# Kernel tuning notes

Measured on AMD Instinct MI355X. Metric: run time of the kernel, lower is better.

The kernel has to match this reference:

```python
import jax, jax.numpy as jnp
import numpy as np

B, S, D_IN, D_OUT = 2, 512, 512, 512
EPS = 1e-5  # torch F.layer_norm default


def _layer_norm_last(x):
    # torch F.layer_norm over last dim, no affine, biased variance
    mu = jnp.mean(x, axis=-1, keepdims=True)
    var = jnp.mean(jnp.square(x - mu), axis=-1, keepdims=True)
    return (x - mu) * jax.lax.rsqrt(var + EPS)


def setup_inputs() -> dict:
    key = jax.random.key(0)
    k_x, k_in, k_out, k_b = jax.random.split(key, 4)
    # torch Linear weights: shape (out_features, in_features), kaiming-uniform-ish scale
    lim = 1.0 / np.sqrt(D_IN)
    x = jax.random.normal(k_x, (B, S, D_IN), dtype=jnp.float32)
    W_in = jax.random.uniform(k_in, (D_IN, D_IN), minval=-lim, maxval=lim, dtype=jnp.float32)
    W_out = jax.random.uniform(k_out, (D_OUT, D_IN), minval=-lim, maxval=lim, dtype=jnp.float32)
    W_b = jax.random.uniform(k_b, (D_OUT, D_IN), minval=-lim, maxval=lim, dtype=jnp.float32)
    return {"x": x, "W_in": W_in, "W_out": W_out, "W_b": W_b}


def reference(x, W_in, W_out, W_b):
    # w1: [B,S,D_in], w2: [B,S,D_out]  (torch Linear: x @ W.T)
    w1 = jnp.einsum('bsd,ed->bse', x, W_in)
    w2 = jnp.einsum('bsd,ed->bse', x, W_out)
    # per-token rank-1 meta weight: [B,S,D_out,D_in]
    w = jnp.einsum('bsi,bsj->bsij', w2, w1)
    w = _layer_norm_last(w)  # normalize each row over in_features
    b = _layer_norm_last(jnp.einsum('bsd,ed->bse', x, W_b))  # [B,S,D_out]
    # batched mat-vec: [B,S,D_out]
    y = jnp.einsum('bsij,bsj->bsi', w, x) + b
    return y
```

## Files before the change

### kernel.cpp

```cpp
#include <hip/hip_runtime.h>
#include <math.h>

#define T_TOK 1024
#define D 512
#define EPS 1e-5f

typedef short bf16x8 __attribute__((ext_vector_type(8)));
typedef float f32x4  __attribute__((ext_vector_type(4)));

__device__ __forceinline__ unsigned short f2bf(float f) {
    unsigned int u = __builtin_bit_cast(unsigned int, f);
    u += 0x7FFFu + ((u >> 16) & 1u);
    return (unsigned short)(u >> 16);
}
__device__ __forceinline__ float bf2f(unsigned short h) {
    return __builtin_bit_cast(float, (unsigned int)h << 16);
}


__global__ __launch_bounds__(256) void convert_kernel(
    const float* __restrict__ X,
    const float* __restrict__ W0,
    const float* __restrict__ W1,
    const float* __restrict__ W2,
    unsigned short* __restrict__ Xh,
    unsigned short* __restrict__ Xl,
    unsigned short* __restrict__ Wh,
    unsigned short* __restrict__ W1l)
{
    constexpr int NX4 = T_TOK * D / 4;
    constexpr int NW4 = D * D / 4;
    const int i = blockIdx.x * 256 + threadIdx.x;

    if (i < NX4) {
        float4 v = reinterpret_cast<const float4*>(X)[i];
        unsigned short h0 = f2bf(v.x), h1 = f2bf(v.y),
                       h2 = f2bf(v.z), h3 = f2bf(v.w);
        ushort4 h = {h0, h1, h2, h3};
        ushort4 l = {f2bf(v.x - bf2f(h0)), f2bf(v.y - bf2f(h1)),
                     f2bf(v.z - bf2f(h2)), f2bf(v.w - bf2f(h3))};
        reinterpret_cast<ushort4*>(Xh)[i] = h;
        reinterpret_cast<ushort4*>(Xl)[i] = l;
    } else {
        int w = i - NX4;
        int z = w / NW4;
        int j = w - z * NW4;
        const float* Wsrc = (z == 0) ? W0 : (z == 1) ? W1 : W2;
        float4 v = reinterpret_cast<const float4*>(Wsrc)[j];
        unsigned short h0 = f2bf(v.x), h1 = f2bf(v.y),
                       h2 = f2bf(v.z), h3 = f2bf(v.w);
        ushort4 h = {h0, h1, h2, h3};
        reinterpret_cast<ushort4*>(Wh)[w] = h;
        if (z == 1) {
            ushort4 l = {f2bf(v.x - bf2f(h0)), f2bf(v.y - bf2f(h1)),
                         f2bf(v.z - bf2f(h2)), f2bf(v.w - bf2f(h3))};
            reinterpret_cast<ushort4*>(W1l)[j] = l;
        }
    }
}

#define LSTR 72

__global__ __launch_bounds__(256) void gemm_bal(
    const unsigned short* __restrict__ Xh,
    const unsigned short* __restrict__ Xl,
    const unsigned short* __restrict__ Wh,
    const unsigned short* __restrict__ W1l,
    float* __restrict__ P)
{
    __shared__ __align__(16) unsigned short SA[2][64 * LSTR];
    __shared__ __align__(16) unsigned short SB[2][64 * LSTR];

    const int tid  = threadIdx.x;
    const int lane = tid & 63;
    const int wid  = tid >> 6;
    const int wr   = wid >> 1;
    const int wc   = wid & 1;
    const int bm   = blockIdx.x * 64;
    const int bn   = blockIdx.y * 64;
    const int z    = blockIdx.z;
    const int l15  = lane & 15;
    const int l4   = lane >> 4;

    const unsigned short* __restrict__ A = (z == 4) ? Xl : Xh;
    const unsigned short* __restrict__ B =
        (z == 3) ? W1l : Wh + (size_t)(z == 4 ? 1 : z) * D * D;

    bf16x8 aP1 = {}, bP1 = {}, aP2 = {}, bP2 = {};
    if (l4 == 0) {
        aP1[0] = (short)f2bf((float)l15);
        bP1[0] = (short)f2bf(1.0f);
        aP2[0] = (short)f2bf(1.0f);
        bP2[0] = (short)f2bf((float)l15);
    }
    f32x4 zero = {};
    f32x4 D1 = __builtin_amdgcn_mfma_f32_16x16x32_bf16(aP1, bP1, zero, 0, 0, 0);
    f32x4 D2 = __builtin_amdgcn_mfma_f32_16x16x32_bf16(aP2, bP2, zero, 0, 0, 0);
    int mi[4], ni[4];
    #pragma unroll
    for (int r = 0; r < 4; ++r) { mi[r] = (int)D1[r]; ni[r] = (int)D2[r]; }

    const int srow = tid >> 3;
    const int scol = (tid & 7) * 8;
    const size_t ga0 = (size_t)(bm + srow) * D + scol;
    const size_t ga1 = (size_t)(bm + srow + 32) * D + scol;
    const size_t gb0 = (size_t)(bn + srow) * D + scol;
    const size_t gb1 = (size_t)(bn + srow + 32) * D + scol;

    f32x4 acc[2][2] = {};
    bf16x8 va0, va1, vb0, vb1;

    va0 = *reinterpret_cast<const bf16x8*>(A + ga0);
    va1 = *reinterpret_cast<const bf16x8*>(A + ga1);
    vb0 = *reinterpret_cast<const bf16x8*>(B + gb0);
    vb1 = *reinterpret_cast<const bf16x8*>(B + gb1);
    *reinterpret_cast<bf16x8*>(&SA[0][srow * LSTR + scol])        = va0;
    *reinterpret_cast<bf16x8*>(&SA[0][(srow + 32) * LSTR + scol]) = va1;
    *reinterpret_cast<bf16x8*>(&SB[0][srow * LSTR + scol])        = vb0;
    *reinterpret_cast<bf16x8*>(&SB[0][(srow + 32) * LSTR + scol]) = vb1;
    __syncthreads();

    int cur = 0;
    #pragma unroll
    for (int t = 0; t < 8; ++t) {
        if (t < 7) {
            const int k0 = (t + 1) * 64;
            va0 = *reinterpret_cast<const bf16x8*>(A + ga0 + k0);
            va1 = *reinterpret_cast<const bf16x8*>(A + ga1 + k0);
            vb0 = *reinterpret_cast<const bf16x8*>(B + gb0 + k0);
            vb1 = *reinterpret_cast<const bf16x8*>(B + gb1 + k0);
        }

        #pragma unroll
        for (int kc = 0; kc < 2; ++kc) {
            const int ko = kc * 32 + l4 * 8;
            bf16x8 a0 = *reinterpret_cast<const bf16x8*>(
                &SA[cur][(wr * 32 + l15) * LSTR + ko]);
            bf16x8 a1 = *reinterpret_cast<const bf16x8*>(
                &SA[cur][(wr * 32 + 16 + l15) * LSTR + ko]);
            bf16x8 b0 = *reinterpret_cast<const bf16x8*>(
                &SB[cur][(wc * 32 + l15) * LSTR + ko]);
            bf16x8 b1 = *reinterpret_cast<const bf16x8*>(
                &SB[cur][(wc * 32 + 16 + l15) * LSTR + ko]);
            acc[0][0] = __builtin_amdgcn_mfma_f32_16x16x32_bf16(a0, b0, acc[0][0], 0, 0, 0);
            acc[0][1] = __builtin_amdgcn_mfma_f32_16x16x32_bf16(a0, b1, acc[0][1], 0, 0, 0);
            acc[1][0] = __builtin_amdgcn_mfma_f32_16x16x32_bf16(a1, b0, acc[1][0], 0, 0, 0);
            acc[1][1] = __builtin_amdgcn_mfma_f32_16x16x32_bf16(a1, b1, acc[1][1], 0, 0, 0);
        }

        if (t < 7) {
            const int nxt = cur ^ 1;
            *reinterpret_cast<bf16x8*>(&SA[nxt][srow * LSTR + scol])        = va0;
            *reinterpret_cast<bf16x8*>(&SA[nxt][(srow + 32) * LSTR + scol]) = va1;
            *reinterpret_cast<bf16x8*>(&SB[nxt][srow * LSTR + scol])        = vb0;
            *reinterpret_cast<bf16x8*>(&SB[nxt][(srow + 32) * LSTR + scol]) = vb1;
            __syncthreads();
            cur = nxt;
        }
    }

    float* __restrict__ Pz = P + (size_t)z * T_TOK * D;
    #pragma unroll
    for (int fm = 0; fm < 2; ++fm)
        #pragma unroll
        for (int fn = 0; fn < 2; ++fn)
            #pragma unroll
            for (int r = 0; r < 4; ++r) {
                int row = bm + wr * 32 + fm * 16 + mi[r];
                int col = bn + wc * 32 + fn * 16 + ni[r];
                Pz[(size_t)row * D + col] = acc[fm][fn][r];
            }
}

__global__ __launch_bounds__(256) void epilogue_kernel(
    const float* __restrict__ X,
    const float* __restrict__ P,
    float* __restrict__ Y)
{
    const int t   = blockIdx.x;
    const int tid = threadIdx.x;
    constexpr size_t SL = (size_t)T_TOK * D;

    const float2* __restrict__ w1 = (const float2*)(P            + (size_t)t * D);
    const float2* __restrict__ p1 = (const float2*)(P + SL       + (size_t)t * D);
    const float2* __restrict__ wb = (const float2*)(P + SL * 2   + (size_t)t * D);
    const float2* __restrict__ p3 = (const float2*)(P + SL * 3   + (size_t)t * D);
    const float2* __restrict__ p4 = (const float2*)(P + SL * 4   + (size_t)t * D);
    const float2* __restrict__ x  = (const float2*)(X            + (size_t)t * D);

    float2 xv  = x[tid];
    float2 w1v = w1[tid];
    float2 wbv = wb[tid];

    float sx  = xv.x + xv.y;
    float s1  = w1v.x + w1v.y;
    float q1  = w1v.x * w1v.x + w1v.y * w1v.y;
    float d1x = w1v.x * xv.x + w1v.y * xv.y;
    float sb  = wbv.x + wbv.y;
    float qb  = wbv.x * wbv.x + wbv.y * wbv.y;

    #pragma unroll
    for (int off = 32; off > 0; off >>= 1) {
        sx  += __shfl_down(sx,  off);
        s1  += __shfl_down(s1,  off);
        q1  += __shfl_down(q1,  off);
        d1x += __shfl_down(d1x, off);
        sb  += __shfl_down(sb,  off);
        qb  += __shfl_down(qb,  off);
    }

    __shared__ float red[6][4];
    const int wave = tid >> 6;
    if ((tid & 63) == 0) {
        red[0][wave] = sx;  red[1][wave] = s1;  red[2][wave] = q1;
        red[3][wave] = d1x; red[4][wave] = sb;  red[5][wave] = qb;
    }
    __syncthreads();
    sx  = red[0][0] + red[0][1] + red[0][2] + red[0][3];
    s1  = red[1][0] + red[1][1] + red[1][2] + red[1][3];
    q1  = red[2][0] + red[2][1] + red[2][2] + red[2][3];
    d1x = red[3][0] + red[3][1] + red[3][2] + red[3][3];
    sb  = red[4][0] + red[4][1] + red[4][2] + red[4][3];
    qb  = red[5][0] + red[5][1] + red[5][2] + red[5][3];

    const float inv_d = 1.f / (float)D;
    const float mu1   = s1 * inv_d;
    const float var1  = q1 * inv_d - mu1 * mu1;
    const float Sv    = d1x - mu1 * sx;
    const float mub   = sb * inv_d;
    const float varb  = qb * inv_d - mub * mub;
    const float rb    = rsqrtf(varb + EPS);

    float2 a = p1[tid], b = p3[tid], c = p4[tid];
    float2 w2v = {a.x + b.x + c.x, a.y + b.y + c.y};
    float2 y;
    y.x = w2v.x * Sv * rsqrtf(w2v.x * w2v.x * var1 + EPS) + (wbv.x - mub) * rb;
    y.y = w2v.y * Sv * rsqrtf(w2v.y * w2v.y * var1 + EPS) + (wbv.y - mub) * rb;
    reinterpret_cast<float2*>(Y + (size_t)t * D)[tid] = y;
}

extern "C" void kernel_launch(void* const* d_in, const int* in_sizes, int n_in,
                              void* d_out, int out_size, void* d_ws, size_t ws_size,
                              hipStream_t stream) {
    const float* x     = (const float*)d_in[0];
    const float* W_in  = (const float*)d_in[1];
    const float* W_out = (const float*)d_in[2];
    const float* W_b   = (const float*)d_in[3];
    float* Y = (float*)d_out;

    char* ws = (char*)d_ws;
    float*          P   = (float*)(ws);
    unsigned short* Xh  = (unsigned short*)(ws + 10485760);
    unsigned short* Xl  = (unsigned short*)(ws + 11534336);
    unsigned short* Wh  = (unsigned short*)(ws + 12582912);
    unsigned short* W1l = (unsigned short*)(ws + 14155776);

    convert_kernel<<<dim3(1280), 256, 0, stream>>>(
        x, W_in, W_out, W_b, Xh, Xl, Wh, W1l);

    gemm_bal<<<dim3(T_TOK / 64, D / 64, 5), 256, 0, stream>>>(
        Xh, Xl, Wh, W1l, P);

    epilogue_kernel<<<dim3(T_TOK), 256, 0, stream>>>(x, P, Y);
}
```

Measured before the change: 24.37 us.

## Fuse fp32-to-bf16 hi/lo conversion into GEMM tile loads, drop convert kernel

Removes the separate conversion kernel and has the GEMM read fp32 X and weights directly, splitting them into bf16 hi or lo parts while staging tiles into shared memory. This saves one kernel launch and the round trip of writing and rereading the bf16 copies. In exchange, each GEMM block loads twice as many bytes per tile (fp32 instead of bf16) and repeats the conversion for every tile it reuses across the grid, which adds VALU work and register pressure inside the main loop.

```diff
diff --git a/kernel.cpp b/kernel.cpp
--- a/kernel.cpp
+++ b/kernel.cpp
@@ -4,6 +4,7 @@
 #define T_TOK 1024
 #define D 512
 #define EPS 1e-5f
+#define LSTR 72
 
 typedef short bf16x8 __attribute__((ext_vector_type(8)));
 typedef float f32x4  __attribute__((ext_vector_type(4)));
@@ -17,55 +18,23 @@
     return __builtin_bit_cast(float, (unsigned int)h << 16);
 }
 
-
-__global__ __launch_bounds__(256) void convert_kernel(
+__device__ __forceinline__ bf16x8 pack8(float4 u0, float4 u1, bool lo) {
+    float v[8] = {u0.x, u0.y, u0.z, u0.w, u1.x, u1.y, u1.z, u1.w};
+    bf16x8 r;
+    #pragma unroll
+    for (int j = 0; j < 8; ++j) {
+        unsigned short h = f2bf(v[j]);
+        r[j] = (short)(lo ? f2bf(v[j] - bf2f(h)) : h);
+    }
+    return r;
+}
+
+
+__global__ __launch_bounds__(256) void gemm_direct(
     const float* __restrict__ X,
     const float* __restrict__ W0,
     const float* __restrict__ W1,
     const float* __restrict__ W2,
-    unsigned short* __restrict__ Xh,
-    unsigned short* __restrict__ Xl,
-    unsigned short* __restrict__ Wh,
-    unsigned short* __restrict__ W1l)
-{
-    constexpr int NX4 = T_TOK * D / 4;
-    constexpr int NW4 = D * D / 4;
-    const int i = blockIdx.x * 256 + threadIdx.x;
-
-    if (i < NX4) {
-        float4 v = reinterpret_cast<const float4*>(X)[i];
-        unsigned short h0 = f2bf(v.x), h1 = f2bf(v.y),
-                       h2 = f2bf(v.z), h3 = f2bf(v.w);
-        ushort4 h = {h0, h1, h2, h3};
-        ushort4 l = {f2bf(v.x - bf2f(h0)), f2bf(v.y - bf2f(h1)),
-                     f2bf(v.z - bf2f(h2)), f2bf(v.w - bf2f(h3))};
-        reinterpret_cast<ushort4*>(Xh)[i] = h;
-        reinterpret_cast<ushort4*>(Xl)[i] = l;
-    } else {
-        int w = i - NX4;
-        int z = w / NW4;
-        int j = w - z * NW4;
-        const float* Wsrc = (z == 0) ? W0 : (z == 1) ? W1 : W2;
-        float4 v = reinterpret_cast<const float4*>(Wsrc)[j];
-        unsigned short h0 = f2bf(v.x), h1 = f2bf(v.y),
-                       h2 = f2bf(v.z), h3 = f2bf(v.w);
-        ushort4 h = {h0, h1, h2, h3};
-        reinterpret_cast<ushort4*>(Wh)[w] = h;
-        if (z == 1) {
-            ushort4 l = {f2bf(v.x - bf2f(h0)), f2bf(v.y - bf2f(h1)),
-                         f2bf(v.z - bf2f(h2)), f2bf(v.w - bf2f(h3))};
-            reinterpret_cast<ushort4*>(W1l)[j] = l;
-        }
-    }
-}
-
-#define LSTR 72
-
-__global__ __launch_bounds__(256) void gemm_bal(
-    const unsigned short* __restrict__ Xh,
-    const unsigned short* __restrict__ Xl,
-    const unsigned short* __restrict__ Wh,
-    const unsigned short* __restrict__ W1l,
     float* __restrict__ P)
 {
     __shared__ __align__(16) unsigned short SA[2][64 * LSTR];
@@ -82,9 +51,9 @@
     const int l15  = lane & 15;
     const int l4   = lane >> 4;
 
-    const unsigned short* __restrict__ A = (z == 4) ? Xl : Xh;
-    const unsigned short* __restrict__ B =
-        (z == 3) ? W1l : Wh + (size_t)(z == 4 ? 1 : z) * D * D;
+    const float* __restrict__ B = (z == 0) ? W0 : (z == 2) ? W2 : W1;
+    const bool alo = (z == 4);
+    const bool blo = (z == 3);
 
     bf16x8 aP1 = {}, bP1 = {}, aP2 = {}, bP2 = {};
     if (l4 == 0) {
@@ -103,21 +72,25 @@
     const int srow = tid >> 3;
     const int scol = (tid & 7) * 8;
     const size_t ga0 = (size_t)(bm + srow) * D + scol;
-    const size_t ga1 = (size_t)(bm + srow + 32) * D + scol;
+    const size_t ga1 = ga0 + (size_t)32 * D;
     const size_t gb0 = (size_t)(bn + srow) * D + scol;
-    const size_t gb1 = (size_t)(bn + srow + 32) * D + scol;
+    const size_t gb1 = gb0 + (size_t)32 * D;
 
     f32x4 acc[2][2] = {};
-    bf16x8 va0, va1, vb0, vb1;
-
-    va0 = *reinterpret_cast<const bf16x8*>(A + ga0);
-    va1 = *reinterpret_cast<const bf16x8*>(A + ga1);
-    vb0 = *reinterpret_cast<const bf16x8*>(B + gb0);
-    vb1 = *reinterpret_cast<const bf16x8*>(B + gb1);
-    *reinterpret_cast<bf16x8*>(&SA[0][srow * LSTR + scol])        = va0;
-    *reinterpret_cast<bf16x8*>(&SA[0][(srow + 32) * LSTR + scol]) = va1;
-    *reinterpret_cast<bf16x8*>(&SB[0][srow * LSTR + scol])        = vb0;
-    *reinterpret_cast<bf16x8*>(&SB[0][(srow + 32) * LSTR + scol]) = vb1;
+    float4 a00, a01, a10, a11, b00, b01, b10, b11;
+
+    a00 = *reinterpret_cast<const float4*>(X + ga0);
+    a01 = *reinterpret_cast<const float4*>(X + ga0 + 4);
+    a10 = *reinterpret_cast<const float4*>(X + ga1);
+    a11 = *reinterpret_cast<const float4*>(X + ga1 + 4);
+    b00 = *reinterpret_cast<const float4*>(B + gb0);
+    b01 = *reinterpret_cast<const float4*>(B + gb0 + 4);
+    b10 = *reinterpret_cast<const float4*>(B + gb1);
+    b11 = *reinterpret_cast<const float4*>(B + gb1 + 4);
+    *reinterpret_cast<bf16x8*>(&SA[0][srow * LSTR + scol])        = pack8(a00, a01, alo);
+    *reinterpret_cast<bf16x8*>(&SA[0][(srow + 32) * LSTR + scol]) = pack8(a10, a11, alo);
+    *reinterpret_cast<bf16x8*>(&SB[0][srow * LSTR + scol])        = pack8(b00, b01, blo);
+    *reinterpret_cast<bf16x8*>(&SB[0][(srow + 32) * LSTR + scol]) = pack8(b10, b11, blo);
     __syncthreads();
 
     int cur = 0;
@@ -125,35 +98,39 @@
     for (int t = 0; t < 8; ++t) {
         if (t < 7) {
             const int k0 = (t + 1) * 64;
-            va0 = *reinterpret_cast<const bf16x8*>(A + ga0 + k0);
-            va1 = *reinterpret_cast<const bf16x8*>(A + ga1 + k0);
-            vb0 = *reinterpret_cast<const bf16x8*>(B + gb0 + k0);
-            vb1 = *reinterpret_cast<const bf16x8*>(B + gb1 + k0);
+            a00 = *reinterpret_cast<const float4*>(X + ga0 + k0);
+            a01 = *reinterpret_cast<const float4*>(X + ga0 + k0 + 4);
+            a10 = *reinterpret_cast<const float4*>(X + ga1 + k0);
+            a11 = *reinterpret_cast<const float4*>(X + ga1 + k0 + 4);
+            b00 = *reinterpret_cast<const float4*>(B + gb0 + k0);
+            b01 = *reinterpret_cast<const float4*>(B + gb0 + k0 + 4);
+            b10 = *reinterpret_cast<const float4*>(B + gb1 + k0);
+            b11 = *reinterpret_cast<const float4*>(B + gb1 + k0 + 4);
         }
 
         #pragma unroll
         for (int kc = 0; kc < 2; ++kc) {
             const int ko = kc * 32 + l4 * 8;
-            bf16x8 a0 = *reinterpret_cast<const bf16x8*>(
+            bf16x8 fa0 = *reinterpret_cast<const bf16x8*>(
                 &SA[cur][(wr * 32 + l15) * LSTR + ko]);
-            bf16x8 a1 = *reinterpret_cast<const bf16x8*>(
+            bf16x8 fa1 = *reinterpret_cast<const bf16x8*>(
                 &SA[cur][(wr * 32 + 16 + l15) * LSTR + ko]);
-            bf16x8 b0 = *reinterpret_cast<const bf16x8*>(
+            bf16x8 fb0 = *reinterpret_cast<const bf16x8*>(
                 &SB[cur][(wc * 32 + l15) * LSTR + ko]);
-            bf16x8 b1 = *reinterpret_cast<const bf16x8*>(
+            bf16x8 fb1 = *reinterpret_cast<const bf16x8*>(
                 &SB[cur][(wc * 32 + 16 + l15) * LSTR + ko]);
-            acc[0][0] = __builtin_amdgcn_mfma_f32_16x16x32_bf16(a0, b0, acc[0][0], 0, 0, 0);
-            acc[0][1] = __builtin_amdgcn_mfma_f32_16x16x32_bf16(a0, b1, acc[0][1], 0, 0, 0);
-            acc[1][0] = __builtin_amdgcn_mfma_f32_16x16x32_bf16(a1, b0, acc[1][0], 0, 0, 0);
-            acc[1][1] = __builtin_amdgcn_mfma_f32_16x16x32_bf16(a1, b1, acc[1][1], 0, 0, 0);
+            acc[0][0] = __builtin_amdgcn_mfma_f32_16x16x32_bf16(fa0, fb0, acc[0][0], 0, 0, 0);
+            acc[0][1] = __builtin_amdgcn_mfma_f32_16x16x32_bf16(fa0, fb1, acc[0][1], 0, 0, 0);
+            acc[1][0] = __builtin_amdgcn_mfma_f32_16x16x32_bf16(fa1, fb0, acc[1][0], 0, 0, 0);
+            acc[1][1] = __builtin_amdgcn_mfma_f32_16x16x32_bf16(fa1, fb1, acc[1][1], 0, 0, 0);
         }
 
         if (t < 7) {
             const int nxt = cur ^ 1;
-            *reinterpret_cast<bf16x8*>(&SA[nxt][srow * LSTR + scol])        = va0;
-            *reinterpret_cast<bf16x8*>(&SA[nxt][(srow + 32) * LSTR + scol]) = va1;
-            *reinterpret_cast<bf16x8*>(&SB[nxt][srow * LSTR + scol])        = vb0;
-            *reinterpret_cast<bf16x8*>(&SB[nxt][(srow + 32) * LSTR + scol]) = vb1;
+            *reinterpret_cast<bf16x8*>(&SA[nxt][srow * LSTR + scol])        = pack8(a00, a01, alo);
+            *reinterpret_cast<bf16x8*>(&SA[nxt][(srow + 32) * LSTR + scol]) = pack8(a10, a11, alo);
+            *reinterpret_cast<bf16x8*>(&SB[nxt][srow * LSTR + scol])        = pack8(b00, b01, blo);
+            *reinterpret_cast<bf16x8*>(&SB[nxt][(srow + 32) * LSTR + scol]) = pack8(b10, b11, blo);
             __syncthreads();
             cur = nxt;
         }
@@ -181,12 +158,12 @@
     const int tid = threadIdx.x;
     constexpr size_t SL = (size_t)T_TOK * D;
 
-    const float2* __restrict__ w1 = (const float2*)(P            + (size_t)t * D);
-    const float2* __restrict__ p1 = (const float2*)(P + SL       + (size_t)t * D);
-    const float2* __restrict__ wb = (const float2*)(P + SL * 2   + (size_t)t * D);
-    const float2* __restrict__ p3 = (const float2*)(P + SL * 3   + (size_t)t * D);
-    const float2* __restrict__ p4 = (const float2*)(P + SL * 4   + (size_t)t * D);
-    const float2* __restrict__ x  = (const float2*)(X            + (size_t)t * D);
+    const float2* __restrict__ w1 = (const float2*)(P          + (size_t)t * D);
+    const float2* __restrict__ p1 = (const float2*)(P + SL     + (size_t)t * D);
+    const float2* __restrict__ wb = (const float2*)(P + SL * 2 + (size_t)t * D);
+    const float2* __restrict__ p3 = (const float2*)(P + SL * 3 + (size_t)t * D);
+    const float2* __restrict__ p4 = (const float2*)(P + SL * 4 + (size_t)t * D);
+    const float2* __restrict__ x  = (const float2*)(X          + (size_t)t * D);
 
     float2 xv  = x[tid];
     float2 w1v = w1[tid];
@@ -247,19 +224,10 @@
     const float* W_out = (const float*)d_in[2];
     const float* W_b   = (const float*)d_in[3];
     float* Y = (float*)d_out;
-
-    char* ws = (char*)d_ws;
-    float*          P   = (float*)(ws);
-    unsigned short* Xh  = (unsigned short*)(ws + 10485760);
-    unsigned short* Xl  = (unsigned short*)(ws + 11534336);
-    unsigned short* Wh  = (unsigned short*)(ws + 12582912);
-    unsigned short* W1l = (unsigned short*)(ws + 14155776);
-
-    convert_kernel<<<dim3(1280), 256, 0, stream>>>(
-        x, W_in, W_out, W_b, Xh, Xl, Wh, W1l);
-
-    gemm_bal<<<dim3(T_TOK / 64, D / 64, 5), 256, 0, stream>>>(
-        Xh, Xl, Wh, W1l, P);
+    float* P = (float*)d_ws;
+
+    gemm_direct<<<dim3(T_TOK / 64, D / 64, 5), 256, 0, stream>>>(
+        x, W_in, W_out, W_b, P);
 
     epilogue_kernel<<<dim3(T_TOK), 256, 0, stream>>>(x, P, Y);
 }
```

Result: faster. 23.42 us (-3.9%).
